# Kernel optimization log

Measured on AMD Instinct MI355X. Metric: run time of the kernel, lower is better.

Reference implementation:

```python
import jax, jax.numpy as jnp
import numpy as np

STEP = 2  # neighbor window size (init arg `step`)


def _shift_sums(x, step):
    # sum over shifted-left (before) and shifted-right (after) neighbor states,
    # zero-padded at the boundaries, for shifts 1..step. x: [B, L, H]
    before = sum(jnp.pad(x[:, :-s, :], ((0, 0), (s, 0), (0, 0))) for s in range(1, step + 1))
    after = sum(jnp.pad(x[:, s:, :], ((0, 0), (0, s), (0, 0))) for s in range(1, step + 1))
    return before, after


def _slstm_forward(word_inputs, mask, num_layers, init_h, init_c, Wx, Wh, Wi, Wd, b, gWx, gWh, gb):
    B, L, D = word_inputs.shape
    H = Wx.shape[-1]
    fm = mask.astype(word_inputs.dtype)          # [B, L]
    seq_mask = fm[:, :, None]                    # [B, L, 1]
    mask_score = (fm * 1e25 - 1e25)[:, :, None]  # -inf-like for padded positions

    emb = word_inputs * seq_mask                 # embedding_hidden_state_pre
    h = (init_h * 0.1 - 0.05) * seq_mask         # uniform(-0.05, 0.05) init
    c = (init_c * 0.1 - 0.05) * seq_mask
    dh = jnp.mean(h, axis=1)                     # dummy-node hidden [B, H]
    dc = jnp.mean(c, axis=1)                     # dummy-node cell   [B, H]

    for _ in range(num_layers):
        comb = jnp.mean(h, axis=1)               # combined word hidden [B, H]
        dh_rep = jnp.broadcast_to(dh[:, None, :], (B, L, H))
        dc_rep = jnp.broadcast_to(dc[:, None, :], (B, L, H))

        # --- dummy (sentence) node update ---
        g_d = jax.nn.sigmoid(dh @ gWx[0] + comb @ gWh[0] + gb[0])              # [B, H]
        g_o = jax.nn.sigmoid(dh @ gWx[1] + comb @ gWh[1] + gb[1])              # [B, H]
        g_f = jax.nn.sigmoid(dh_rep @ gWx[2] + h @ gWh[2] + gb[2])             # [B, L, H]
        scores = jnp.concatenate([g_f + mask_score, g_d[:, None, :]], axis=1)  # [B, L+1, H]
        scores = jax.nn.softmax(scores, axis=1)
        dummy_c = jnp.sum(scores[:, :L, :] * c, axis=1) + scores[:, L, :] * dc
        dummy_h = g_o * jnp.tanh(dummy_c)

        # --- word node updates ---
        hb, ha = _shift_sums(h, STEP)
        cb, ca = _shift_sums(c, STEP)
        cat_h = jnp.concatenate([hb, ha], axis=-1)  # [B, L, 2H]

        # 7 gates stacked: f1, f2, f3, f4, i, o, u -> pre: [7, B, L, H]
        pre = (jnp.einsum('blh,ghk->gblk', h, Wx)
               + jnp.einsum('blh,ghk->gblk', cat_h, Wh)
               + jnp.einsum('bld,gdk->gblk', emb, Wi)
               + jnp.einsum('blh,ghk->gblk', dh_rep, Wd)
               + b[:, None, None, :])
        sig = jax.nn.sigmoid(pre[:6])
        f1, f2, f3, f4, i_g, o_g = sig[0], sig[1], sig[2], sig[3], sig[4], sig[5]
        u = jnp.tanh(pre[6])

        # normalize the five forget/input gates via softmax across gates
        five = jax.nn.softmax(jnp.stack([f1, f2, f3, f4, i_g], axis=0), axis=0)
        c_new = five[0] * cb + five[1] * ca + five[2] * c + five[3] * dc_rep + five[4] * u
        h_new = o_g * jnp.tanh(c_new)

        h = h_new * seq_mask
        c = c_new * seq_mask
        dh, dc = dummy_h, dummy_c

    return h


def setup_inputs() -> dict:
    key = jax.random.key(0)
    ks = jax.random.split(key, 12)
    B, L, D, H, G = 32, 1024, 256, 256, 7
    s = 0.1  # stddev of param init in the torch module
    return {
        'word_inputs': jax.random.normal(ks[0], (B, L, D), jnp.float32),
        'mask': jnp.ones((B, L), jnp.int32),
        'num_layers': 3,
        'init_h': jax.random.uniform(ks[1], (B, L, H), jnp.float32),
        'init_c': jax.random.uniform(ks[2], (B, L, H), jnp.float32),
        'Wx': jax.random.normal(ks[3], (G, H, H), jnp.float32) * s,
        'Wh': jax.random.normal(ks[4], (G, 2 * H, H), jnp.float32) * s,
        'Wi': jax.random.normal(ks[5], (G, D, H), jnp.float32) * s,
        'Wd': jax.random.normal(ks[6], (G, H, H), jnp.float32) * s,
        'b': jax.random.normal(ks[7], (G, H), jnp.float32) * s,
        'gWx': jax.random.normal(ks[8], (3, H, H), jnp.float32) * s,
        'gWh': jax.random.normal(ks[9], (3, H, H), jnp.float32) * s,
        'gb': jax.random.normal(ks[10], (3, H), jnp.float32) * s,
    }


def reference(word_inputs, mask, num_layers, init_h, init_c, Wx, Wh, Wi, Wd, b, gWx, gWh, gb):
    return _slstm_forward(word_inputs, mask, num_layers, init_h, init_c, Wx, Wh, Wi, Wd, b, gWx, gWh, gb)
```

## Files before the change

### kernel.cpp

```cpp
#include <hip/hip_runtime.h>
#include <hip/hip_bf16.h>
#include <math.h>

#define BB 32
#define LL 1024
#define DD 256
#define HH 256
#define NG 7
#define HW (HH*HH)
#define WhS (2*HH*HH)

typedef short bf16x8 __attribute__((ext_vector_type(8)));
typedef float f32x4  __attribute__((ext_vector_type(4)));
typedef unsigned short u16;
typedef unsigned int u32;

__device__ __forceinline__ float sigm(float x){ return 1.0f/(1.0f + expf(-x)); }
__device__ __forceinline__ float fsig(float x){ return __fdividef(1.0f, 1.0f + __expf(-x)); }
__device__ __forceinline__ float ftanh(float x){ return 1.0f - __fdividef(2.0f, 1.0f + __expf(2.0f*x)); }
__device__ __forceinline__ u16 f2b(float f){
  u32 u = __float_as_uint(f);
  return (u16)((u + 0x7fffu + ((u>>16)&1u)) >> 16);
}
__device__ __forceinline__ float b2f(u16 b){ return __uint_as_float(((u32)b)<<16); }
__device__ __forceinline__ float4 ld4(const float* p){ return *reinterpret_cast<const float4*>(p); }
__device__ __forceinline__ u32 packf2(float lo, float hi){
  float2 s; s.x = lo; s.y = hi;
  __hip_bfloat162 r = __float22bfloat162_rn(s);
  return *reinterpret_cast<u32*>(&r);
}
__device__ __forceinline__ u32 bfadd2(u32 a, u32 b){
  float lo = __uint_as_float(a << 16)        + __uint_as_float(b << 16);
  float hi = __uint_as_float(a & 0xffff0000u) + __uint_as_float(b & 0xffff0000u);
  return packf2(lo, hi);
}

__device__ __forceinline__ void gload16(const void* g, void* l){
  __builtin_amdgcn_global_load_lds(
    (const __attribute__((address_space(1))) unsigned int*)g,
    (__attribute__((address_space(3))) unsigned int*)l, 16, 0, 0);
}
__device__ __forceinline__ f32x4 mfma16(bf16x8 a, bf16x8 b, f32x4 c){
  return __builtin_amdgcn_mfma_f32_16x16x32_bf16(a, b, c, 0, 0, 0);
}

__global__ __launch_bounds__(256) void k_init(const float* __restrict__ ih, const float* __restrict__ ic,
    const int* __restrict__ mask, u16* __restrict__ h, float* __restrict__ c,
    float* __restrict__ pmh, float* __restrict__ pmc){
  int b = blockIdx.x, ch = blockIdx.y, k = threadIdx.x;
  size_t base = ((size_t)b*LL + ch*64)*HH + k;
  float sh = 0.f, sc = 0.f;
  for (int l = 0; l < 64; ++l){
    size_t idx = base + (size_t)l*HH;
    float fm = (float)mask[b*LL + ch*64 + l];
    float hv = (ih[idx]*0.1f - 0.05f)*fm;
    float cv = (ic[idx]*0.1f - 0.05f)*fm;
    h[idx] = f2b(hv);
    c[idx] = cv;
    sh += hv; sc += cv;
  }
  pmh[(size_t)(b*16+ch)*HH + k] = sh;
  pmc[(size_t)(b*16+ch)*HH + k] = sc;
}

__global__ __launch_bounds__(256) void k_embpack(const float* __restrict__ win,
    const int* __restrict__ mask, u16* __restrict__ embp){
  int idx = blockIdx.x*256 + threadIdx.x;
  int m = idx >> 5, c8 = (idx & 31) << 3;
  float fm = (float)mask[m];
  float4 w0 = ld4(win + (size_t)m*DD + c8);
  float4 w1 = ld4(win + (size_t)m*DD + c8 + 4);
  uint4 pv;
  pv.x = packf2(w0.x*fm, w0.y*fm); pv.y = packf2(w0.z*fm, w0.w*fm);
  pv.z = packf2(w1.x*fm, w1.y*fm); pv.w = packf2(w1.z*fm, w1.w*fm);
  *(uint4*)(embp + (size_t)m*HH + c8) = pv;
}

__global__ __launch_bounds__(256) void k_ms(const float* __restrict__ pmh, const float* __restrict__ pmc,
    const float* __restrict__ dh_in,
    const float* __restrict__ gWx, const float* __restrict__ gWh, const float* __restrict__ gb,
    const float* __restrict__ Wd, const float* __restrict__ bias,
    float* __restrict__ g_d, float* __restrict__ g_o, float* __restrict__ gx2f, float* __restrict__ wd,
    float* __restrict__ combc_out, int l0flag){
  __shared__ float dsh[HH], csh[HH];
  int b = blockIdx.x, g = blockIdx.y, k = threadIdx.x;
  float sh = 0.f;
  for (int ch = 0; ch < 16; ++ch) sh += pmh[(size_t)(b*16+ch)*HH + k];
  float comb = sh*(1.0f/LL);
  csh[k] = comb;
  dsh[k] = l0flag ? comb : dh_in[b*HH+k];
  __syncthreads();
  if (g < NG){
    float aw = bias[g*HH+k];
    const float* W = Wd + (size_t)g*HW + k;
    for (int j = 0; j < HH; ++j) aw += dsh[j]*W[(size_t)j*HH];
    wd[(size_t)(g*BB + b)*HH + k] = aw;
  } else {
    float ad = gb[0*HH+k], ao = gb[1*HH+k], ax = gb[2*HH+k];
    for (int j = 0; j < HH; ++j){
      float dv = dsh[j], cv = csh[j];
      ad += dv*gWx[j*HH+k]      + cv*gWh[j*HH+k];
      ao += dv*gWx[HW + j*HH+k] + cv*gWh[HW + j*HH+k];
      ax += dv*gWx[2*HW + j*HH+k];
    }
    g_d[b*HH+k] = sigm(ad);
    g_o[b*HH+k] = sigm(ao);
    gx2f[b*HH+k] = ax;
    if (l0flag){
      float sc = 0.f;
      for (int ch = 0; ch < 16; ++ch) sc += pmc[(size_t)(b*16+ch)*HH + k];
      combc_out[b*HH+k] = sc*(1.0f/LL);
    }
  }
}

__global__ __launch_bounds__(256) void k_wpack(const float* __restrict__ Wx, const float* __restrict__ Wh,
    const float* __restrict__ Wi, u16* __restrict__ Bp){
  int idx = blockIdx.x*256 + threadIdx.x;
  int img = idx / 14336, e = idx % 14336;
  int nt = img >> 5, ks = img & 31;
  int g = e >> 11, r = e & 2047;
  int n = r >> 5, kblk = (r>>3)&3, j = r&7;
  int K = ks*32 + kblk*8 + j;
  int N = nt*64 + n;
  int slice = K >> 8, kr = K & 255;
  float v;
  if (slice == 0)      v = Wx[(size_t)g*HW  + (size_t)kr*HH + N];
  else if (slice == 1) v = Wh[(size_t)g*WhS + (size_t)kr*HH + N];
  else if (slice == 2) v = Wh[(size_t)g*WhS + (size_t)(256+kr)*HH + N];
  else                 v = Wi[(size_t)g*HW  + (size_t)kr*HH + N];
  Bp[idx] = f2b(v);
}

__global__ __launch_bounds__(256) void k_gw2pack(const float* __restrict__ gWh, u16* __restrict__ Gp){
  int idx = blockIdx.x*256 + threadIdx.x;
  int img = idx >> 11, r = idx & 2047;
  int nt = img >> 3, ks = img & 7;
  int n = r >> 5, kblk = (r>>3)&3, j = r&7;
  int K = ks*32 + kblk*8 + j, N = nt*64 + n;
  Gp[idx] = f2b(gWh[2*HW + (size_t)K*HH + N]);
}

__global__ __launch_bounds__(256) void k_dummy2(const float* __restrict__ pnumP, const float* __restrict__ pdenP,
    const float* __restrict__ g_d, const float* __restrict__ g_o, const float* __restrict__ dc,
    float* __restrict__ dh_n, float* __restrict__ dc_n){
  int b = blockIdx.x, k = threadIdx.x;
  float num = 0.f, den = 0.f;
  for (int mt = 0; mt < 16; ++mt){
    num += pnumP[(size_t)(b*16+mt)*HH + k];
    den += pdenP[(size_t)(b*16+mt)*HH + k];
  }
  float ed = expf(g_d[b*HH+k]);
  float v = (num + ed*dc[b*HH+k])/(den + ed);
  dc_n[b*HH+k] = v;
  dh_n[b*HH+k] = g_o[b*HH+k]*tanhf(v);
}

__global__ __launch_bounds__(256, 2) void k_main(const u16* __restrict__ h,
    const float* __restrict__ c, const u16* __restrict__ embp,
    const int* __restrict__ mask,
    const u16* __restrict__ Bp, const u16* __restrict__ Gp,
    const float* __restrict__ wd, const float* __restrict__ dc,
    const float* __restrict__ gx2f,
    u16* __restrict__ hout, float* __restrict__ cout, float* __restrict__ hf32,
    float* __restrict__ pnumP, float* __restrict__ pdenP,
    float* __restrict__ pmh, float* __restrict__ pmc, int wf32, int wc){
  __shared__ __align__(16) unsigned char lsA[3][4][4096];

  int tid = threadIdx.x, lane = tid & 63, wid = tid >> 6;
  int flat = blockIdx.x;
  int xcd = flat & 7, q = flat >> 3;
  int nt  = xcd >> 1;
  int mt  = (xcd & 1)*256 + q;
  int m0 = mt << 6, b = m0 >> 10;
  int li = lane & 15, kg = lane >> 4;

  int kbA = (lane&3) ^ ((lane>>3)&3);
  int mA = m0 + wid*16 + (lane>>2), lpA = mA & (LL-1);

  int off0 = li*64 + ((kg ^ ((li>>1)&3))<<4);

  const unsigned char* bbase = (const unsigned char*)Bp
      + (size_t)nt*32*28672 + (size_t)(wid*16+li)*64 + (size_t)kg*16;
  const unsigned char* gbase = (const unsigned char*)Gp
      + (size_t)nt*8*4096  + (size_t)(wid*16+li)*64 + (size_t)kg*16;

  f32x4 acc[NG][4];
  f32x4 acc8[4];
  #pragma unroll
  for (int g=0; g<NG; ++g)
    #pragma unroll
    for (int mf=0; mf<4; ++mf) acc[g][mf] = (f32x4)0.f;
  #pragma unroll
  for (int mf=0; mf<4; ++mf) acc8[mf] = (f32x4)0.f;

  auto stage = [&](int Gs, int dst){
    int base = 4*Gs, s1 = base >> 3;
    if (s1 == 0 || s1 == 3){
      const u16* src = (s1 == 0) ? h : embp;
      #pragma unroll
      for (int j=0;j<4;++j)
        gload16(src + (size_t)mA*HH + ((base+j)&7)*32 + kbA*8, lsA[dst][j] + wid*1024);
    } else {
      int d = (s1 == 1) ? -(int)HH : (int)HH;
      bool e1 = (s1 == 1) ? (lpA >= 1) : (lpA <= LL-2);
      bool e2 = (s1 == 1) ? (lpA >= 2) : (lpA <= LL-3);
      #pragma unroll
      for (int j=0;j<4;++j){
        int co = ((base+j)&7)*32 + kbA*8;
        const u16* hp = h + (size_t)mA*HH + co;
        uint4 u1 = e1 ? *(const uint4*)(hp + d)   : make_uint4(0,0,0,0);
        uint4 u2 = e2 ? *(const uint4*)(hp + 2*d) : make_uint4(0,0,0,0);
        uint4 pv;
        pv.x = bfadd2(u1.x,u2.x); pv.y = bfadd2(u1.y,u2.y);
        pv.z = bfadd2(u1.z,u2.z); pv.w = bfadd2(u1.w,u2.w);
        *(uint4*)(lsA[dst][j] + wid*1024 + lane*16) = pv;
      }
    }
  };

  stage(0, 0);
  stage(1, 1);
  asm volatile("s_waitcnt vmcnt(4)" ::: "memory");
  __builtin_amdgcn_s_barrier();

  #pragma unroll 1
  for (int G = 0; G < 8; ++G){
    if (G < 6) stage(G+2, (G+2)%3);
    int setc = G % 3;
    #pragma unroll
    for (int j = 0; j < 4; ++j){
      int ks = 4*G + j;
      const unsigned char* bstep = bbase + (size_t)ks*28672;
      bf16x8 bg[NG];
      #pragma unroll
      for (int g = 0; g < NG; ++g) bg[g] = *(const bf16x8*)(bstep + g*4096);
      bf16x8 aa[4];
      #pragma unroll
      for (int mf=0; mf<4; ++mf)
        aa[mf] = *(const bf16x8*)(lsA[setc][j] + mf*1024 + off0);
      __builtin_amdgcn_s_setprio(1);
      #pragma unroll
      for (int g = 0; g < NG; ++g)
        #pragma unroll
        for (int mf=0; mf<4; ++mf) acc[g][mf] = mfma16(aa[mf], bg[g], acc[g][mf]);
      if (ks < 8){
        bf16x8 b8 = *(const bf16x8*)(gbase + (size_t)ks*4096);
        #pragma unroll
        for (int mf=0; mf<4; ++mf) acc8[mf] = mfma16(aa[mf], b8, acc8[mf]);
      }
      __builtin_amdgcn_s_setprio(0);
    }
    asm volatile("s_waitcnt vmcnt(4)" ::: "memory");
    __builtin_amdgcn_s_barrier();
  }

  int col = nt*64 + wid*16 + li;
  float wdv[NG];
  #pragma unroll
  for (int g=0; g<NG; ++g) wdv[g] = wd[(size_t)(g*BB+b)*HH + col];
  float dcv = dc[b*HH + col];
  float gx  = gx2f[b*HH + col];
  float num = 0.f, den = 0.f, msh = 0.f, msc = 0.f;

  #pragma unroll
  for (int mf=0; mf<4; ++mf)
  #pragma unroll
  for (int j=0; j<4; ++j){
    int m = m0 + mf*16 + kg*4 + j;
    int lp = m & (LL-1);
    float fm = (float)mask[m];
    const float* cp = c + (size_t)m*HH + col;
    float cc = cp[0];
    float cbv = 0.f, cav = 0.f;
    if (lp >= 1)    cbv += cp[-(int)HH];
    if (lp >= 2)    cbv += cp[-2*(int)HH];
    if (lp <= LL-2) cav += cp[HH];
    if (lp <= LL-3) cav += cp[2*HH];
    float s0 = fsig(acc[0][mf][j] + wdv[0]);
    float s1 = fsig(acc[1][mf][j] + wdv[1]);
    float s2 = fsig(acc[2][mf][j] + wdv[2]);
    float s3 = fsig(acc[3][mf][j] + wdv[3]);
    float s4 = fsig(acc[4][mf][j] + wdv[4]);
    float s5 = fsig(acc[5][mf][j] + wdv[5]);
    float u  = ftanh(acc[6][mf][j] + wdv[6]);
    float e0 = __expf(s0), e1 = __expf(s1), e2 = __expf(s2), e3 = __expf(s3), e4 = __expf(s4);
    float inv = __fdividef(1.0f, e0+e1+e2+e3+e4);
    float cn = (e0*cbv + e1*cav + e2*cc + e3*dcv + e4*u)*inv;
    float hn = s5*ftanh(cn);
    float ho = hn*fm, co = cn*fm;
    hout[(size_t)m*HH + col] = f2b(ho);
    if (wc)   cout[(size_t)m*HH + col] = co;
    if (wf32) hf32[(size_t)m*HH + col] = ho;
    float s8 = fsig(acc8[mf][j] + gx);
    float e8 = fm * __expf(s8);
    num += e8 * cc;
    den += e8;
    msh += ho; msc += co;
  }
  num += __shfl_xor(num, 16); num += __shfl_xor(num, 32);
  den += __shfl_xor(den, 16); den += __shfl_xor(den, 32);
  msh += __shfl_xor(msh, 16); msh += __shfl_xor(msh, 32);
  msc += __shfl_xor(msc, 16); msc += __shfl_xor(msc, 32);
  if (kg == 0){
    size_t tix = (size_t)(m0>>6)*HH + col;
    pnumP[tix] = num;
    pdenP[tix] = den;
    pmh[tix]   = msh;
    pmc[tix]   = msc;
  }
}

extern "C" void kernel_launch(void* const* d_in, const int* in_sizes, int n_in,
                              void* d_out, int out_size, void* d_ws, size_t ws_size,
                              hipStream_t stream) {
  const float* win   = (const float*)d_in[0];
  const int*   mask  = (const int*)d_in[1];
  const float* ih    = (const float*)d_in[3];
  const float* ic    = (const float*)d_in[4];
  const float* Wx    = (const float*)d_in[5];
  const float* Wh    = (const float*)d_in[6];
  const float* Wi    = (const float*)d_in[7];
  const float* Wd    = (const float*)d_in[8];
  const float* bias  = (const float*)d_in[9];
  const float* gWx   = (const float*)d_in[10];
  const float* gWh   = (const float*)d_in[11];
  const float* gb    = (const float*)d_in[12];

  const size_t SZ = (size_t)BB*LL*HH;
  char* p = (char*)d_ws;
  auto alloc = [&](size_t bytes)->char*{ char* r = p; p += (bytes + 255) & ~(size_t)255; return r; };
  u16*   hA    = (u16*)  alloc(SZ*2);
  u16*   hB    = (u16*)  alloc(SZ*2);
  float* cA    = (float*)alloc(SZ*4);
  float* cB    = (float*)d_out;
  u16*   embp  = (u16*)  alloc(SZ*2);
  u16*   Bp    = (u16*)  alloc((size_t)1835008*2);
  u16*   Gp    = (u16*)  alloc((size_t)65536*2);
  float* combc = (float*)alloc(BB*HH*4);
  float* dh0   = (float*)alloc(BB*HH*4);
  float* dh1   = (float*)alloc(BB*HH*4);
  float* dc0   = (float*)alloc(BB*HH*4);
  float* dc1   = (float*)alloc(BB*HH*4);
  float* g_d   = (float*)alloc(BB*HH*4);
  float* g_o   = (float*)alloc(BB*HH*4);
  float* gx2f  = (float*)alloc(BB*HH*4);
  float* wd    = (float*)alloc((size_t)NG*BB*HH*4);
  float* pnumP = (float*)alloc((size_t)512*HH*4);
  float* pdenP = (float*)alloc((size_t)512*HH*4);
  float* pmh   = (float*)alloc((size_t)512*HH*4);
  float* pmc   = (float*)alloc((size_t)512*HH*4);
  float* dhb[2] = {dh0, dh1};
  float* dcb[2] = {dc0, dc1};

  k_wpack<<<7168, 256, 0, stream>>>(Wx, Wh, Wi, Bp);
  k_gw2pack<<<256, 256, 0, stream>>>(gWh, Gp);
  k_embpack<<<4096, 256, 0, stream>>>(win, mask, embp);
  k_init<<<dim3(BB,16), 256, 0, stream>>>(ih, ic, mask, hA, cA, pmh, pmc);

  u16 *h_cur = hA, *h_nxt = hB;
  float *c_cur = cA, *c_nxt = cB;
  for (int layer = 0; layer < 3; ++layer){
    int l0 = (layer == 0);
    const float* dh_l = l0 ? (const float*)nullptr : dhb[(layer+1)&1];
    const float* dc_l = l0 ? combc : dcb[(layer+1)&1];
    k_ms<<<dim3(BB,8), 256, 0, stream>>>(pmh, pmc, dh_l, gWx, gWh, gb, Wd, bias,
                                         g_d, g_o, gx2f, wd, combc, l0);
    int last = (layer == 2);
    k_main<<<2048, 256, 0, stream>>>(h_cur, c_cur, embp, mask, Bp, Gp, wd, dc_l, gx2f,
                                     h_nxt, c_nxt, (float*)d_out, pnumP, pdenP,
                                     pmh, pmc, last, !last);
    k_dummy2<<<BB, 256, 0, stream>>>(pnumP, pdenP, g_d, g_o, dc_l, dhb[layer&1], dcb[layer&1]);
    u16* th = h_cur; h_cur = h_nxt; h_nxt = th;
    float* tc = c_cur; c_cur = c_nxt; c_nxt = tc;
  }
}
```

Baseline: 665.9 us.

## Precompute shifted neighbor sums per layer and stage embeddings in-kernel

Adds a per-layer k_shift kernel that materialises the before/after neighbor sums of h into bf16 buffers, so the GEMM's A-tile staging for those K-slices becomes plain async global-to-LDS loads. The embedding pre-pack kernel is removed; k_main now reads fp32 inputs, applies the mask and converts to bf16 while staging. Staging of the next tile moves after the MFMA loop, and the waits also drain LDS counters. This removes register-path loads of four neighbor rows from the main loop, but costs an extra write and read of two h-sized buffers per layer and doubles the bytes read for the embedding slice.

```diff
diff --git a/kernel.cpp b/kernel.cpp
--- a/kernel.cpp
+++ b/kernel.cpp
@@ -63,17 +63,23 @@
   pmc[(size_t)(b*16+ch)*HH + k] = sc;
 }
 
-__global__ __launch_bounds__(256) void k_embpack(const float* __restrict__ win,
-    const int* __restrict__ mask, u16* __restrict__ embp){
+__global__ __launch_bounds__(256) void k_shift(const u16* __restrict__ h,
+    u16* __restrict__ hb, u16* __restrict__ ha){
   int idx = blockIdx.x*256 + threadIdx.x;
-  int m = idx >> 5, c8 = (idx & 31) << 3;
-  float fm = (float)mask[m];
-  float4 w0 = ld4(win + (size_t)m*DD + c8);
-  float4 w1 = ld4(win + (size_t)m*DD + c8 + 4);
-  uint4 pv;
-  pv.x = packf2(w0.x*fm, w0.y*fm); pv.y = packf2(w0.z*fm, w0.w*fm);
-  pv.z = packf2(w1.x*fm, w1.y*fm); pv.w = packf2(w1.z*fm, w1.w*fm);
-  *(uint4*)(embp + (size_t)m*HH + c8) = pv;
+  int row = idx >> 5, c8 = (idx & 31) << 3;
+  int l = row & (LL-1);
+  const u16* hp = h + (size_t)row*HH + c8;
+  uint4 u1 = (l >= 1)    ? *(const uint4*)(hp - HH)   : make_uint4(0,0,0,0);
+  uint4 u2 = (l >= 2)    ? *(const uint4*)(hp - 2*HH) : make_uint4(0,0,0,0);
+  uint4 v1 = (l <= LL-2) ? *(const uint4*)(hp + HH)   : make_uint4(0,0,0,0);
+  uint4 v2 = (l <= LL-3) ? *(const uint4*)(hp + 2*HH) : make_uint4(0,0,0,0);
+  uint4 pb, pa;
+  pb.x = bfadd2(u1.x,u2.x); pb.y = bfadd2(u1.y,u2.y);
+  pb.z = bfadd2(u1.z,u2.z); pb.w = bfadd2(u1.w,u2.w);
+  pa.x = bfadd2(v1.x,v2.x); pa.y = bfadd2(v1.y,v2.y);
+  pa.z = bfadd2(v1.z,v2.z); pa.w = bfadd2(v1.w,v2.w);
+  *(uint4*)(hb + (size_t)row*HH + c8) = pb;
+  *(uint4*)(ha + (size_t)row*HH + c8) = pa;
 }
 
 __global__ __launch_bounds__(256) void k_ms(const float* __restrict__ pmh, const float* __restrict__ pmc,
@@ -157,7 +163,8 @@
 }
 
 __global__ __launch_bounds__(256, 2) void k_main(const u16* __restrict__ h,
-    const float* __restrict__ c, const u16* __restrict__ embp,
+    const u16* __restrict__ hb, const u16* __restrict__ ha,
+    const float* __restrict__ c, const float* __restrict__ win,
     const int* __restrict__ mask,
     const u16* __restrict__ Bp, const u16* __restrict__ Gp,
     const float* __restrict__ wd, const float* __restrict__ dc,
@@ -176,7 +183,8 @@
   int li = lane & 15, kg = lane >> 4;
 
   int kbA = (lane&3) ^ ((lane>>3)&3);
-  int mA = m0 + wid*16 + (lane>>2), lpA = mA & (LL-1);
+  int mA = m0 + wid*16 + (lane>>2);
+  float fmA = (float)mask[mA];
 
   int off0 = li*64 + ((kg ^ ((li>>1)&3))<<4);
 
@@ -196,24 +204,20 @@
 
   auto stage = [&](int Gs, int dst){
     int base = 4*Gs, s1 = base >> 3;
-    if (s1 == 0 || s1 == 3){
-      const u16* src = (s1 == 0) ? h : embp;
+    if (s1 < 3){
+      const u16* src = (s1==0) ? h : (s1==1) ? hb : ha;
       #pragma unroll
       for (int j=0;j<4;++j)
         gload16(src + (size_t)mA*HH + ((base+j)&7)*32 + kbA*8, lsA[dst][j] + wid*1024);
     } else {
-      int d = (s1 == 1) ? -(int)HH : (int)HH;
-      bool e1 = (s1 == 1) ? (lpA >= 1) : (lpA <= LL-2);
-      bool e2 = (s1 == 1) ? (lpA >= 2) : (lpA <= LL-3);
       #pragma unroll
       for (int j=0;j<4;++j){
         int co = ((base+j)&7)*32 + kbA*8;
-        const u16* hp = h + (size_t)mA*HH + co;
-        uint4 u1 = e1 ? *(const uint4*)(hp + d)   : make_uint4(0,0,0,0);
-        uint4 u2 = e2 ? *(const uint4*)(hp + 2*d) : make_uint4(0,0,0,0);
+        float4 w0 = ld4(win + (size_t)mA*DD + co);
+        float4 w1 = ld4(win + (size_t)mA*DD + co + 4);
         uint4 pv;
-        pv.x = bfadd2(u1.x,u2.x); pv.y = bfadd2(u1.y,u2.y);
-        pv.z = bfadd2(u1.z,u2.z); pv.w = bfadd2(u1.w,u2.w);
+        pv.x = packf2(w0.x*fmA, w0.y*fmA); pv.y = packf2(w0.z*fmA, w0.w*fmA);
+        pv.z = packf2(w1.x*fmA, w1.y*fmA); pv.w = packf2(w1.z*fmA, w1.w*fmA);
         *(uint4*)(lsA[dst][j] + wid*1024 + lane*16) = pv;
       }
     }
@@ -221,12 +225,11 @@
 
   stage(0, 0);
   stage(1, 1);
-  asm volatile("s_waitcnt vmcnt(4)" ::: "memory");
+  asm volatile("s_waitcnt vmcnt(4) lgkmcnt(0)" ::: "memory");
   __builtin_amdgcn_s_barrier();
 
   #pragma unroll 1
   for (int G = 0; G < 8; ++G){
-    if (G < 6) stage(G+2, (G+2)%3);
     int setc = G % 3;
     #pragma unroll
     for (int j = 0; j < 4; ++j){
@@ -251,7 +254,8 @@
       }
       __builtin_amdgcn_s_setprio(0);
     }
-    asm volatile("s_waitcnt vmcnt(4)" ::: "memory");
+    if (G < 6) stage(G+2, (G+2)%3);
+    asm volatile("s_waitcnt vmcnt(4) lgkmcnt(0)" ::: "memory");
     __builtin_amdgcn_s_barrier();
   }
 
@@ -334,7 +338,8 @@
   u16*   hB    = (u16*)  alloc(SZ*2);
   float* cA    = (float*)alloc(SZ*4);
   float* cB    = (float*)d_out;
-  u16*   embp  = (u16*)  alloc(SZ*2);
+  u16*   hbbuf = (u16*)  alloc(SZ*2);
+  u16*   habuf = (u16*)  alloc(SZ*2);
   u16*   Bp    = (u16*)  alloc((size_t)1835008*2);
   u16*   Gp    = (u16*)  alloc((size_t)65536*2);
   float* combc = (float*)alloc(BB*HH*4);
@@ -355,7 +360,6 @@
 
   k_wpack<<<7168, 256, 0, stream>>>(Wx, Wh, Wi, Bp);
   k_gw2pack<<<256, 256, 0, stream>>>(gWh, Gp);
-  k_embpack<<<4096, 256, 0, stream>>>(win, mask, embp);
   k_init<<<dim3(BB,16), 256, 0, stream>>>(ih, ic, mask, hA, cA, pmh, pmc);
 
   u16 *h_cur = hA, *h_nxt = hB;
@@ -364,10 +368,12 @@
     int l0 = (layer == 0);
     const float* dh_l = l0 ? (const float*)nullptr : dhb[(layer+1)&1];
     const float* dc_l = l0 ? combc : dcb[(layer+1)&1];
+    k_shift<<<4096, 256, 0, stream>>>(h_cur, hbbuf, habuf);
     k_ms<<<dim3(BB,8), 256, 0, stream>>>(pmh, pmc, dh_l, gWx, gWh, gb, Wd, bias,
                                          g_d, g_o, gx2f, wd, combc, l0);
     int last = (layer == 2);
-    k_main<<<2048, 256, 0, stream>>>(h_cur, c_cur, embp, mask, Bp, Gp, wd, dc_l, gx2f,
+    k_main<<<2048, 256, 0, stream>>>(h_cur, hbbuf, habuf, c_cur, win, mask, Bp, Gp,
+                                     wd, dc_l, gx2f,
                                      h_nxt, c_nxt, (float*)d_out, pnumP, pdenP,
                                      pmh, pmc, last, !last);
     k_dummy2<<<BB, 256, 0, stream>>>(pnumP, pdenP, g_d, g_o, dc_l, dhb[layer&1], dcb[layer&1]);
```

Measured after the change: 681.6 us. 2.4% more time.

## Load A operands directly into registers and fuse embedding packing into main kernel

Applied to the files above, without the earlier changes.

Removes the LDS triple-buffered staging of the activation tile (global_load_lds plus barriers). Each wave now loads its A fragments straight from global memory into registers, and the shifted-neighbor sums are computed on the fly. The separate embedding pack kernel is dropped: k_main reads the fp32 word inputs, applies the mask and converts to bf16 inline. This saves a launch, a bf16 buffer and the LDS and sync overhead. In exchange, every wave issues redundant global loads, since the four waves share the same A rows, and the software pipelining across k-steps is lost. The fp32 embedding read is also done three times, once per layer.

```diff
diff --git a/kernel.cpp b/kernel.cpp
--- a/kernel.cpp
+++ b/kernel.cpp
@@ -33,12 +33,6 @@
   float lo = __uint_as_float(a << 16)        + __uint_as_float(b << 16);
   float hi = __uint_as_float(a & 0xffff0000u) + __uint_as_float(b & 0xffff0000u);
   return packf2(lo, hi);
-}
-
-__device__ __forceinline__ void gload16(const void* g, void* l){
-  __builtin_amdgcn_global_load_lds(
-    (const __attribute__((address_space(1))) unsigned int*)g,
-    (__attribute__((address_space(3))) unsigned int*)l, 16, 0, 0);
 }
 __device__ __forceinline__ f32x4 mfma16(bf16x8 a, bf16x8 b, f32x4 c){
   return __builtin_amdgcn_mfma_f32_16x16x32_bf16(a, b, c, 0, 0, 0);
@@ -61,19 +55,6 @@
   }
   pmh[(size_t)(b*16+ch)*HH + k] = sh;
   pmc[(size_t)(b*16+ch)*HH + k] = sc;
-}
-
-__global__ __launch_bounds__(256) void k_embpack(const float* __restrict__ win,
-    const int* __restrict__ mask, u16* __restrict__ embp){
-  int idx = blockIdx.x*256 + threadIdx.x;
-  int m = idx >> 5, c8 = (idx & 31) << 3;
-  float fm = (float)mask[m];
-  float4 w0 = ld4(win + (size_t)m*DD + c8);
-  float4 w1 = ld4(win + (size_t)m*DD + c8 + 4);
-  uint4 pv;
-  pv.x = packf2(w0.x*fm, w0.y*fm); pv.y = packf2(w0.z*fm, w0.w*fm);
-  pv.z = packf2(w1.x*fm, w1.y*fm); pv.w = packf2(w1.z*fm, w1.w*fm);
-  *(uint4*)(embp + (size_t)m*HH + c8) = pv;
 }
 
 __global__ __launch_bounds__(256) void k_ms(const float* __restrict__ pmh, const float* __restrict__ pmc,
@@ -157,7 +138,7 @@
 }
 
 __global__ __launch_bounds__(256, 2) void k_main(const u16* __restrict__ h,
-    const float* __restrict__ c, const u16* __restrict__ embp,
+    const float* __restrict__ c, const float* __restrict__ win,
     const int* __restrict__ mask,
     const u16* __restrict__ Bp, const u16* __restrict__ Gp,
     const float* __restrict__ wd, const float* __restrict__ dc,
@@ -165,8 +146,6 @@
     u16* __restrict__ hout, float* __restrict__ cout, float* __restrict__ hf32,
     float* __restrict__ pnumP, float* __restrict__ pdenP,
     float* __restrict__ pmh, float* __restrict__ pmc, int wf32, int wc){
-  __shared__ __align__(16) unsigned char lsA[3][4][4096];
-
   int tid = threadIdx.x, lane = tid & 63, wid = tid >> 6;
   int flat = blockIdx.x;
   int xcd = flat & 7, q = flat >> 3;
@@ -175,10 +154,20 @@
   int m0 = mt << 6, b = m0 >> 10;
   int li = lane & 15, kg = lane >> 4;
 
-  int kbA = (lane&3) ^ ((lane>>3)&3);
-  int mA = m0 + wid*16 + (lane>>2), lpA = mA & (LL-1);
-
-  int off0 = li*64 + ((kg ^ ((li>>1)&3))<<4);
+  const u16*   hrow[4];
+  const float* wrow[4];
+  float fmr[4];
+  bool ge1[4], ge2[4], le2[4], le3[4];
+  #pragma unroll
+  for (int mf=0; mf<4; ++mf){
+    int m = m0 + mf*16 + li;
+    int lp = m & (LL-1);
+    hrow[mf] = h   + (size_t)m*HH + kg*8;
+    wrow[mf] = win + (size_t)m*DD + kg*8;
+    fmr[mf] = (float)mask[m];
+    ge1[mf] = (lp >= 1);    ge2[mf] = (lp >= 2);
+    le2[mf] = (lp <= LL-2); le3[mf] = (lp <= LL-3);
+  }
 
   const unsigned char* bbase = (const unsigned char*)Bp
       + (size_t)nt*32*28672 + (size_t)(wid*16+li)*64 + (size_t)kg*16;
@@ -194,65 +183,66 @@
   #pragma unroll
   for (int mf=0; mf<4; ++mf) acc8[mf] = (f32x4)0.f;
 
-  auto stage = [&](int Gs, int dst){
-    int base = 4*Gs, s1 = base >> 3;
-    if (s1 == 0 || s1 == 3){
-      const u16* src = (s1 == 0) ? h : embp;
-      #pragma unroll
-      for (int j=0;j<4;++j)
-        gload16(src + (size_t)mA*HH + ((base+j)&7)*32 + kbA*8, lsA[dst][j] + wid*1024);
+  const uint4 Z = make_uint4(0,0,0,0);
+
+  #pragma unroll
+  for (int ks = 0; ks < 32; ++ks){
+    const int slice = ks >> 3;
+    const int cb = (ks & 7) * 32;
+    bf16x8 aa[4];
+    if (slice == 0){
+      #pragma unroll
+      for (int mf=0; mf<4; ++mf)
+        aa[mf] = *(const bf16x8*)(hrow[mf] + cb);
+    } else if (slice == 1){
+      #pragma unroll
+      for (int mf=0; mf<4; ++mf){
+        const u16* p = hrow[mf] + cb;
+        uint4 u1 = ge1[mf] ? *(const uint4*)(p - HH)   : Z;
+        uint4 u2 = ge2[mf] ? *(const uint4*)(p - 2*HH) : Z;
+        uint4 s;
+        s.x = bfadd2(u1.x,u2.x); s.y = bfadd2(u1.y,u2.y);
+        s.z = bfadd2(u1.z,u2.z); s.w = bfadd2(u1.w,u2.w);
+        aa[mf] = *reinterpret_cast<bf16x8*>(&s);
+      }
+    } else if (slice == 2){
+      #pragma unroll
+      for (int mf=0; mf<4; ++mf){
+        const u16* p = hrow[mf] + cb;
+        uint4 u1 = le2[mf] ? *(const uint4*)(p + HH)   : Z;
+        uint4 u2 = le3[mf] ? *(const uint4*)(p + 2*HH) : Z;
+        uint4 s;
+        s.x = bfadd2(u1.x,u2.x); s.y = bfadd2(u1.y,u2.y);
+        s.z = bfadd2(u1.z,u2.z); s.w = bfadd2(u1.w,u2.w);
+        aa[mf] = *reinterpret_cast<bf16x8*>(&s);
+      }
     } else {
-      int d = (s1 == 1) ? -(int)HH : (int)HH;
-      bool e1 = (s1 == 1) ? (lpA >= 1) : (lpA <= LL-2);
-      bool e2 = (s1 == 1) ? (lpA >= 2) : (lpA <= LL-3);
-      #pragma unroll
-      for (int j=0;j<4;++j){
-        int co = ((base+j)&7)*32 + kbA*8;
-        const u16* hp = h + (size_t)mA*HH + co;
-        uint4 u1 = e1 ? *(const uint4*)(hp + d)   : make_uint4(0,0,0,0);
-        uint4 u2 = e2 ? *(const uint4*)(hp + 2*d) : make_uint4(0,0,0,0);
-        uint4 pv;
-        pv.x = bfadd2(u1.x,u2.x); pv.y = bfadd2(u1.y,u2.y);
-        pv.z = bfadd2(u1.z,u2.z); pv.w = bfadd2(u1.w,u2.w);
-        *(uint4*)(lsA[dst][j] + wid*1024 + lane*16) = pv;
+      #pragma unroll
+      for (int mf=0; mf<4; ++mf){
+        const float* wp = wrow[mf] + cb;
+        float4 w0 = ld4(wp), w1 = ld4(wp + 4);
+        float fm = fmr[mf];
+        uint4 s;
+        s.x = packf2(w0.x*fm, w0.y*fm); s.y = packf2(w0.z*fm, w0.w*fm);
+        s.z = packf2(w1.x*fm, w1.y*fm); s.w = packf2(w1.z*fm, w1.w*fm);
+        aa[mf] = *reinterpret_cast<bf16x8*>(&s);
       }
     }
-  };
-
-  stage(0, 0);
-  stage(1, 1);
-  asm volatile("s_waitcnt vmcnt(4)" ::: "memory");
-  __builtin_amdgcn_s_barrier();
-
-  #pragma unroll 1
-  for (int G = 0; G < 8; ++G){
-    if (G < 6) stage(G+2, (G+2)%3);
-    int setc = G % 3;
+    const unsigned char* bstep = bbase + (size_t)ks*28672;
+    bf16x8 bg[NG];
     #pragma unroll
-    for (int j = 0; j < 4; ++j){
-      int ks = 4*G + j;
-      const unsigned char* bstep = bbase + (size_t)ks*28672;
-      bf16x8 bg[NG];
-      #pragma unroll
-      for (int g = 0; g < NG; ++g) bg[g] = *(const bf16x8*)(bstep + g*4096);
-      bf16x8 aa[4];
-      #pragma unroll
-      for (int mf=0; mf<4; ++mf)
-        aa[mf] = *(const bf16x8*)(lsA[setc][j] + mf*1024 + off0);
-      __builtin_amdgcn_s_setprio(1);
-      #pragma unroll
-      for (int g = 0; g < NG; ++g)
-        #pragma unroll
-        for (int mf=0; mf<4; ++mf) acc[g][mf] = mfma16(aa[mf], bg[g], acc[g][mf]);
-      if (ks < 8){
-        bf16x8 b8 = *(const bf16x8*)(gbase + (size_t)ks*4096);
-        #pragma unroll
-        for (int mf=0; mf<4; ++mf) acc8[mf] = mfma16(aa[mf], b8, acc8[mf]);
-      }
-      __builtin_amdgcn_s_setprio(0);
+    for (int g = 0; g < NG; ++g) bg[g] = *(const bf16x8*)(bstep + g*4096);
+    __builtin_amdgcn_s_setprio(1);
+    #pragma unroll
+    for (int g = 0; g < NG; ++g)
+      #pragma unroll
+      for (int mf=0; mf<4; ++mf) acc[g][mf] = mfma16(aa[mf], bg[g], acc[g][mf]);
+    if (ks < 8){
+      bf16x8 b8 = *(const bf16x8*)(gbase + (size_t)ks*4096);
+      #pragma unroll
+      for (int mf=0; mf<4; ++mf) acc8[mf] = mfma16(aa[mf], b8, acc8[mf]);
     }
-    asm volatile("s_waitcnt vmcnt(4)" ::: "memory");
-    __builtin_amdgcn_s_barrier();
+    __builtin_amdgcn_s_setprio(0);
   }
 
   int col = nt*64 + wid*16 + li;
@@ -334,7 +324,6 @@
   u16*   hB    = (u16*)  alloc(SZ*2);
   float* cA    = (float*)alloc(SZ*4);
   float* cB    = (float*)d_out;
-  u16*   embp  = (u16*)  alloc(SZ*2);
   u16*   Bp    = (u16*)  alloc((size_t)1835008*2);
   u16*   Gp    = (u16*)  alloc((size_t)65536*2);
   float* combc = (float*)alloc(BB*HH*4);
@@ -355,7 +344,6 @@
 
   k_wpack<<<7168, 256, 0, stream>>>(Wx, Wh, Wi, Bp);
   k_gw2pack<<<256, 256, 0, stream>>>(gWh, Gp);
-  k_embpack<<<4096, 256, 0, stream>>>(win, mask, embp);
   k_init<<<dim3(BB,16), 256, 0, stream>>>(ih, ic, mask, hA, cA, pmh, pmc);
 
   u16 *h_cur = hA, *h_nxt = hB;
@@ -367,7 +355,8 @@
     k_ms<<<dim3(BB,8), 256, 0, stream>>>(pmh, pmc, dh_l, gWx, gWh, gb, Wd, bias,
                                          g_d, g_o, gx2f, wd, combc, l0);
     int last = (layer == 2);
-    k_main<<<2048, 256, 0, stream>>>(h_cur, c_cur, embp, mask, Bp, Gp, wd, dc_l, gx2f,
+    k_main<<<2048, 256, 0, stream>>>(h_cur, c_cur, win, mask, Bp, Gp,
+                                     wd, dc_l, gx2f,
                                      h_nxt, c_nxt, (float*)d_out, pnumP, pdenP,
                                      pmh, pmc, last, !last);
     k_dummy2<<<BB, 256, 0, stream>>>(pnumP, pdenP, g_d, g_o, dc_l, dhb[layer&1], dcb[layer&1]);
```

Result: slower. 1.352 ms (+103.1%).

## Split fused gate GEMM into two passes to cut accumulators and raise occupancy

Applied to the files above, without the earlier changes.

The 8-gate fused main kernel is split into two template passes. The first computes four gate pre-activations and writes them to a bf16 scratch buffer. The second computes the remaining three gates plus the dummy-node gate, then reads the first pass's results back for the epilogue. Each pass holds only 4 accumulator groups instead of 8, so launch bounds allow 3 blocks per CU instead of 2. The price is that the A-operand staging (h, shifted sums, embeddings) is read twice, plus an extra bf16 round trip of about 64 MB per layer and one more kernel launch. The two-pass path is used only when the workspace is large enough.

```diff
diff --git a/kernel.cpp b/kernel.cpp
--- a/kernel.cpp
+++ b/kernel.cpp
@@ -156,6 +156,187 @@
   dh_n[b*HH+k] = g_o[b*HH+k]*tanhf(v);
 }
 
+template<int PASS>
+__global__ __launch_bounds__(256, 3) void k_mainP(const u16* __restrict__ h,
+    const float* __restrict__ c, const u16* __restrict__ embp,
+    const int* __restrict__ mask,
+    const u16* __restrict__ Bp, const u16* __restrict__ Gp,
+    const float* __restrict__ wd, const float* __restrict__ dc,
+    const float* __restrict__ gx2f, ushort4* __restrict__ pre4,
+    u16* __restrict__ hout, float* __restrict__ cout, float* __restrict__ hf32,
+    float* __restrict__ pnumP, float* __restrict__ pdenP,
+    float* __restrict__ pmh, float* __restrict__ pmc, int wf32, int wc){
+  __shared__ __align__(16) unsigned char lsA[3][4][4096];
+
+  int tid = threadIdx.x, lane = tid & 63, wid = tid >> 6;
+  int flat = blockIdx.x;
+  int xcd = flat & 7, q = flat >> 3;
+  int nt  = xcd >> 1;
+  int mt  = (xcd & 1)*256 + q;
+  int m0 = mt << 6, b = m0 >> 10;
+  int li = lane & 15, kg = lane >> 4;
+
+  int kbA = (lane&3) ^ ((lane>>3)&3);
+  int mA = m0 + wid*16 + (lane>>2), lpA = mA & (LL-1);
+  int off0 = li*64 + ((kg ^ ((li>>1)&3))<<4);
+
+  const unsigned char* bbase = (const unsigned char*)Bp
+      + (size_t)nt*32*28672 + (size_t)(wid*16+li)*64 + (size_t)kg*16;
+  const unsigned char* gbase = (const unsigned char*)Gp
+      + (size_t)nt*8*4096  + (size_t)(wid*16+li)*64 + (size_t)kg*16;
+
+  f32x4 acc[4][4];
+  #pragma unroll
+  for (int u=0; u<4; ++u)
+    #pragma unroll
+    for (int mf=0; mf<4; ++mf) acc[u][mf] = (f32x4)0.f;
+
+  auto stage = [&](int Gs, int dst){
+    int base = 4*Gs, s1 = base >> 3;
+    if (s1 == 0 || s1 == 3){
+      const u16* src = (s1 == 0) ? h : embp;
+      #pragma unroll
+      for (int j=0;j<4;++j)
+        gload16(src + (size_t)mA*HH + ((base+j)&7)*32 + kbA*8, lsA[dst][j] + wid*1024);
+    } else {
+      int d = (s1 == 1) ? -(int)HH : (int)HH;
+      bool e1 = (s1 == 1) ? (lpA >= 1) : (lpA <= LL-2);
+      bool e2 = (s1 == 1) ? (lpA >= 2) : (lpA <= LL-3);
+      #pragma unroll
+      for (int j=0;j<4;++j){
+        int co = ((base+j)&7)*32 + kbA*8;
+        const u16* hp = h + (size_t)mA*HH + co;
+        uint4 u1 = e1 ? *(const uint4*)(hp + d)   : make_uint4(0,0,0,0);
+        uint4 u2 = e2 ? *(const uint4*)(hp + 2*d) : make_uint4(0,0,0,0);
+        uint4 pv;
+        pv.x = bfadd2(u1.x,u2.x); pv.y = bfadd2(u1.y,u2.y);
+        pv.z = bfadd2(u1.z,u2.z); pv.w = bfadd2(u1.w,u2.w);
+        *(uint4*)(lsA[dst][j] + wid*1024 + lane*16) = pv;
+      }
+    }
+  };
+
+  stage(0, 0);
+  stage(1, 1);
+  asm volatile("s_waitcnt vmcnt(4)" ::: "memory");
+  __builtin_amdgcn_s_barrier();
+
+  #pragma unroll 1
+  for (int G = 0; G < 8; ++G){
+    if (G < 6) stage(G+2, (G+2)%3);
+    int setc = G % 3;
+    #pragma unroll
+    for (int j = 0; j < 4; ++j){
+      int ks = 4*G + j;
+      const unsigned char* bstep = bbase + (size_t)ks*28672;
+      bf16x8 aa[4];
+      #pragma unroll
+      for (int mf=0; mf<4; ++mf)
+        aa[mf] = *(const bf16x8*)(lsA[setc][j] + mf*1024 + off0);
+      if (PASS == 0){
+        bf16x8 bg[4];
+        #pragma unroll
+        for (int g = 0; g < 4; ++g) bg[g] = *(const bf16x8*)(bstep + (size_t)g*4096);
+        __builtin_amdgcn_s_setprio(1);
+        #pragma unroll
+        for (int g = 0; g < 4; ++g)
+          #pragma unroll
+          for (int mf=0; mf<4; ++mf) acc[g][mf] = mfma16(aa[mf], bg[g], acc[g][mf]);
+        __builtin_amdgcn_s_setprio(0);
+      } else {
+        bf16x8 bg[3];
+        #pragma unroll
+        for (int g = 0; g < 3; ++g) bg[g] = *(const bf16x8*)(bstep + (size_t)(4+g)*4096);
+        bf16x8 b8;
+        if (ks < 8) b8 = *(const bf16x8*)(gbase + (size_t)ks*4096);
+        __builtin_amdgcn_s_setprio(1);
+        #pragma unroll
+        for (int g = 0; g < 3; ++g)
+          #pragma unroll
+          for (int mf=0; mf<4; ++mf) acc[g][mf] = mfma16(aa[mf], bg[g], acc[g][mf]);
+        if (ks < 8){
+          #pragma unroll
+          for (int mf=0; mf<4; ++mf) acc[3][mf] = mfma16(aa[mf], b8, acc[3][mf]);
+        }
+        __builtin_amdgcn_s_setprio(0);
+      }
+    }
+    asm volatile("s_waitcnt vmcnt(4)" ::: "memory");
+    __builtin_amdgcn_s_barrier();
+  }
+
+  int col = nt*64 + wid*16 + li;
+
+  if (PASS == 0){
+    #pragma unroll
+    for (int mf=0; mf<4; ++mf)
+      #pragma unroll
+      for (int j=0; j<4; ++j){
+        int m = m0 + mf*16 + kg*4 + j;
+        ushort4 pv;
+        pv.x = f2b(acc[0][mf][j]); pv.y = f2b(acc[1][mf][j]);
+        pv.z = f2b(acc[2][mf][j]); pv.w = f2b(acc[3][mf][j]);
+        pre4[(size_t)m*HH + col] = pv;
+      }
+    return;
+  }
+
+  float wdv[NG];
+  #pragma unroll
+  for (int g=0; g<NG; ++g) wdv[g] = wd[(size_t)(g*BB+b)*HH + col];
+  float dcv = dc[b*HH + col];
+  float gx  = gx2f[b*HH + col];
+  float num = 0.f, den = 0.f, msh = 0.f, msc = 0.f;
+
+  #pragma unroll
+  for (int mf=0; mf<4; ++mf)
+  #pragma unroll
+  for (int j=0; j<4; ++j){
+    int m = m0 + mf*16 + kg*4 + j;
+    int lp = m & (LL-1);
+    float fm = (float)mask[m];
+    const float* cp = c + (size_t)m*HH + col;
+    float cc = cp[0];
+    float cbv = 0.f, cav = 0.f;
+    if (lp >= 1)    cbv += cp[-(int)HH];
+    if (lp >= 2)    cbv += cp[-2*(int)HH];
+    if (lp <= LL-2) cav += cp[HH];
+    if (lp <= LL-3) cav += cp[2*HH];
+    ushort4 pv = pre4[(size_t)m*HH + col];
+    float s0 = fsig(b2f(pv.x) + wdv[0]);
+    float s1 = fsig(b2f(pv.y) + wdv[1]);
+    float s2 = fsig(b2f(pv.z) + wdv[2]);
+    float s3 = fsig(b2f(pv.w) + wdv[3]);
+    float s4 = fsig(acc[0][mf][j] + wdv[4]);
+    float s5 = fsig(acc[1][mf][j] + wdv[5]);
+    float u  = ftanh(acc[2][mf][j] + wdv[6]);
+    float e0 = __expf(s0), e1 = __expf(s1), e2 = __expf(s2), e3 = __expf(s3), e4 = __expf(s4);
+    float inv = __fdividef(1.0f, e0+e1+e2+e3+e4);
+    float cn = (e0*cbv + e1*cav + e2*cc + e3*dcv + e4*u)*inv;
+    float hn = s5*ftanh(cn);
+    float ho = hn*fm, co = cn*fm;
+    hout[(size_t)m*HH + col] = f2b(ho);
+    if (wc)   cout[(size_t)m*HH + col] = co;
+    if (wf32) hf32[(size_t)m*HH + col] = ho;
+    float s8 = fsig(acc[3][mf][j] + gx);
+    float e8 = fm * __expf(s8);
+    num += e8 * cc;
+    den += e8;
+    msh += ho; msc += co;
+  }
+  num += __shfl_xor(num, 16); num += __shfl_xor(num, 32);
+  den += __shfl_xor(den, 16); den += __shfl_xor(den, 32);
+  msh += __shfl_xor(msh, 16); msh += __shfl_xor(msh, 32);
+  msc += __shfl_xor(msc, 16); msc += __shfl_xor(msc, 32);
+  if (kg == 0){
+    size_t tix = (size_t)(m0>>6)*HH + col;
+    pnumP[tix] = num;
+    pdenP[tix] = den;
+    pmh[tix]   = msh;
+    pmc[tix]   = msc;
+  }
+}
+
 __global__ __launch_bounds__(256, 2) void k_main(const u16* __restrict__ h,
     const float* __restrict__ c, const u16* __restrict__ embp,
     const int* __restrict__ mask,
@@ -177,7 +358,6 @@
 
   int kbA = (lane&3) ^ ((lane>>3)&3);
   int mA = m0 + wid*16 + (lane>>2), lpA = mA & (LL-1);
-
   int off0 = li*64 + ((kg ^ ((li>>1)&3))<<4);
 
   const unsigned char* bbase = (const unsigned char*)Bp
@@ -350,6 +530,9 @@
   float* pdenP = (float*)alloc((size_t)512*HH*4);
   float* pmh   = (float*)alloc((size_t)512*HH*4);
   float* pmc   = (float*)alloc((size_t)512*HH*4);
+  ushort4* pre4 = (ushort4*)alloc(SZ*8);
+  size_t used = (size_t)(p - (char*)d_ws);
+  int two_pass = (used <= ws_size);
   float* dhb[2] = {dh0, dh1};
   float* dcb[2] = {dc0, dc1};
 
@@ -367,9 +550,18 @@
     k_ms<<<dim3(BB,8), 256, 0, stream>>>(pmh, pmc, dh_l, gWx, gWh, gb, Wd, bias,
                                          g_d, g_o, gx2f, wd, combc, l0);
     int last = (layer == 2);
-    k_main<<<2048, 256, 0, stream>>>(h_cur, c_cur, embp, mask, Bp, Gp, wd, dc_l, gx2f,
-                                     h_nxt, c_nxt, (float*)d_out, pnumP, pdenP,
-                                     pmh, pmc, last, !last);
+    if (two_pass){
+      k_mainP<0><<<2048, 256, 0, stream>>>(h_cur, c_cur, embp, mask, Bp, Gp, wd, dc_l, gx2f,
+                                           pre4, h_nxt, c_nxt, (float*)d_out, pnumP, pdenP,
+                                           pmh, pmc, last, !last);
+      k_mainP<1><<<2048, 256, 0, stream>>>(h_cur, c_cur, embp, mask, Bp, Gp, wd, dc_l, gx2f,
+                                           pre4, h_nxt, c_nxt, (float*)d_out, pnumP, pdenP,
+                                           pmh, pmc, last, !last);
+    } else {
+      k_main<<<2048, 256, 0, stream>>>(h_cur, c_cur, embp, mask, Bp, Gp, wd, dc_l, gx2f,
+                                       h_nxt, c_nxt, (float*)d_out, pnumP, pdenP,
+                                       pmh, pmc, last, !last);
+    }
     k_dummy2<<<BB, 256, 0, stream>>>(pnumP, pdenP, g_d, g_o, dc_l, dhb[layer&1], dcb[layer&1]);
     u16* th = h_cur; h_cur = h_nxt; h_nxt = th;
     float* tc = c_cur; c_cur = c_nxt; c_nxt = tc;
```

After: 769.0 us. +15.5%, slower.
